# Performance work log

Hardware: AMD Instinct MI355X
Metric: run time of the kernel (lower is better)

Reference implementation:

```python
import jax, jax.numpy as jnp
import numpy as np
import math

B, S, D, H = 2, 2048, 1024, 16
DK = D // H


def setup_inputs() -> dict:
    key = jax.random.key(0)
    ks = jax.random.split(key, 10)
    sc = 1.0 / math.sqrt(D)
    inp = {
        "Q_input": jax.random.normal(ks[0], (B, S, D), dtype=jnp.float32),
        "Wq_w": jax.random.normal(ks[1], (D, D), dtype=jnp.float32) * sc,
        "Wq_b": jnp.zeros((D,), dtype=jnp.float32),
        "Wk_w": jax.random.normal(ks[2], (D, D), dtype=jnp.float32) * sc,
        "Wk_b": jnp.zeros((D,), dtype=jnp.float32),
        "Wv_w": jax.random.normal(ks[3], (D, D), dtype=jnp.float32) * sc,
        "Wv_b": jnp.zeros((D,), dtype=jnp.float32),
        "Wo_w": jax.random.normal(ks[4], (D, D), dtype=jnp.float32) * sc,
        "Wo_b": jnp.zeros((D,), dtype=jnp.float32),
        # causal mask, broadcast over batch and heads: [1,1,S,S]
        "mask": jnp.tril(jnp.ones((S, S), dtype=jnp.int32))[None, None],
    }
    return inp


def reference(Q_input, Wq_w, Wq_b, Wk_w, Wk_b, Wv_w, Wv_b, Wo_w, Wo_b, mask):
    b, s, _ = Q_input.shape
    # linear projections (torch Linear: x @ W^T + b)
    Q = Q_input @ Wq_w.T + Wq_b
    K = Q_input @ Wk_w.T + Wk_b
    V = Q_input @ Wv_w.T + Wv_b
    # [b, h, s, dk]
    Q = Q.reshape(b, s, H, DK).transpose(0, 2, 1, 3)
    K = K.reshape(b, s, H, DK).transpose(0, 2, 1, 3)
    V = V.reshape(b, s, H, DK).transpose(0, 2, 1, 3)
    scores = jnp.einsum("bhqd,bhkd->bhqk", Q, K) / math.sqrt(DK)
    scores = jnp.where(mask == 0, jnp.float32(-1e9), scores)
    weights = jax.nn.softmax(scores, axis=-1)
    attn = jnp.einsum("bhqk,bhkd->bhqd", weights, V)
    attn = attn.transpose(0, 2, 1, 3).reshape(b, s, D)
    return attn @ Wo_w.T + Wo_b
```

## Files before the change

kernel.cpp:

```cpp
#include <hip/hip_runtime.h>
#include <hip/hip_bf16.h>
#include <cstdint>

typedef __attribute__((ext_vector_type(8))) short short8;
typedef __attribute__((ext_vector_type(4))) float f32x4;
typedef __attribute__((ext_vector_type(2))) unsigned int uint2v;
typedef unsigned short ushort_t;

#define S_LEN 2048
#define D_DIM 1024
#define NH 16
#define DK 64
#define BATCH 2
#define M_ROWS (BATCH * S_LEN)
#define BK 32

__device__ inline ushort_t f2bf(float f) {
    union { float f; uint32_t u; } v; v.f = f;
    uint32_t r = v.u + 0x7fffu + ((v.u >> 16) & 1u);
    return (ushort_t)(r >> 16);
}

__device__ __forceinline__ ushort_t bfc(float f) {
    __hip_bfloat16 h = __float2bfloat16(f);
    return __builtin_bit_cast(ushort_t, h);
}

__device__ __forceinline__ void glds16(const ushort_t* g, ushort_t* l) {
    __builtin_amdgcn_global_load_lds(
        (const __attribute__((address_space(1))) uint32_t*)g,
        (__attribute__((address_space(3))) uint32_t*)l,
        16, 0, 0);
}

#if __has_builtin(__builtin_amdgcn_permlane16_swap) && __has_builtin(__builtin_amdgcn_permlane32_swap)
#define HAS_PLSWAP 1
#else
#define HAS_PLSWAP 0
#endif

__device__ __forceinline__ float red_max4(float x) {
#if HAS_PLSWAP
    uint2v a = __builtin_amdgcn_permlane16_swap(__float_as_uint(x), __float_as_uint(x), false, false);
    float y = fmaxf(__uint_as_float(a.x), __uint_as_float(a.y));
    uint2v b = __builtin_amdgcn_permlane32_swap(__float_as_uint(y), __float_as_uint(y), false, false);
    return fmaxf(__uint_as_float(b.x), __uint_as_float(b.y));
#else
    x = fmaxf(x, __shfl_xor(x, 16));
    return fmaxf(x, __shfl_xor(x, 32));
#endif
}
__device__ __forceinline__ float red_sum4(float x) {
#if HAS_PLSWAP
    uint2v a = __builtin_amdgcn_permlane16_swap(__float_as_uint(x), __float_as_uint(x), false, false);
    float y = __uint_as_float(a.x) + __uint_as_float(a.y);
    uint2v b = __builtin_amdgcn_permlane32_swap(__float_as_uint(y), __float_as_uint(y), false, false);
    return __uint_as_float(b.x) + __uint_as_float(b.y);
#else
    x += __shfl_xor(x, 16);
    return x + __shfl_xor(x, 32);
#endif
}

__device__ __forceinline__ void route_p(const uint32_t wp[4][2], int ks, int lane, uint32_t F[4]) {
#if HAS_PLSWAP
    uint32_t U0 = wp[2 * ks][0],     U1 = wp[2 * ks][1];
    uint32_t V0 = wp[2 * ks + 1][0], V1 = wp[2 * ks + 1][1];
    uint2v t, pa0, pa1, pb0, pb1;
    t = __builtin_amdgcn_permlane32_swap(U0, U0, false, false);
    pa0 = __builtin_amdgcn_permlane16_swap(U0, t.y, false, false);
    t = __builtin_amdgcn_permlane32_swap(U1, U1, false, false);
    pa1 = __builtin_amdgcn_permlane16_swap(U1, t.y, false, false);
    t = __builtin_amdgcn_permlane32_swap(V0, V0, false, false);
    pb0 = __builtin_amdgcn_permlane16_swap(t.x, V0, false, false);
    t = __builtin_amdgcn_permlane32_swap(V1, V1, false, false);
    pb1 = __builtin_amdgcn_permlane16_swap(t.x, V1, false, false);
    bool lo = lane < 32;
    F[0] = lo ? pa0.x : pb0.x;
    F[1] = lo ? pa1.x : pb1.x;
    F[2] = lo ? pa0.y : pb0.y;
    F[3] = lo ? pa1.y : pb1.y;
#else
    int q = lane & 15, g = lane >> 4;
#pragma unroll
    for (int m = 0; m < 4; m++) {
        int src = 16 * (2 * (g & 1) + (m >> 1)) + q;
        uint32_t xa = (uint32_t)__shfl((int)wp[2 * ks][m & 1], src);
        uint32_t xb = (uint32_t)__shfl((int)wp[2 * ks + 1][m & 1], src);
        F[m] = (g < 2) ? xa : xb;
    }
#endif
}

__global__ void cvt_bf16(const float* __restrict__ in, ushort_t* __restrict__ out, int n4) {
    int i = blockIdx.x * blockDim.x + threadIdx.x;
    int stride = gridDim.x * blockDim.x;
    for (int idx = i; idx < n4; idx += stride) {
        float4 v = ((const float4*)in)[idx];
        ushort4 o;
        o.x = f2bf(v.x); o.y = f2bf(v.y); o.z = f2bf(v.z); o.w = f2bf(v.w);
        ((ushort4*)out)[idx] = o;
    }
}

__global__ void cvt_w3(const float* __restrict__ wq, const float* __restrict__ wk,
                       const float* __restrict__ wv, ushort_t* __restrict__ wqkv) {
    const int seg = (D_DIM * D_DIM) / 4;
    int i = blockIdx.x * blockDim.x + threadIdx.x;
    int stride = gridDim.x * blockDim.x;
    for (int idx = i; idx < 3 * seg; idx += stride) {
        int sel = idx >> 18;
        int id = idx & (seg - 1);
        const float* src = sel == 0 ? wq : (sel == 1 ? wk : wv);
        float4 v = ((const float4*)src)[id];
        ushort4 o;
        o.x = f2bf(v.x); o.y = f2bf(v.y); o.z = f2bf(v.z); o.w = f2bf(v.w);
        ((ushort4*)wqkv)[sel * seg + id] = o;
    }
}

template<int MODE, int BMt, int BNt>
__global__ __launch_bounds__(256) void gemm_bt(const ushort_t* __restrict__ A,
                                               const ushort_t* __restrict__ Bw,
                                               const float* __restrict__ b0,
                                               const float* __restrict__ b1,
                                               const float* __restrict__ b2,
                                               void* __restrict__ C0,
                                               void* __restrict__ C1,
                                               void* __restrict__ C2,
                                               int M, int N, int K) {
    constexpr int FM = BMt / 32, FN = BNt / 32;
    constexpr int ACH = BMt / 64, BCH = BNt / 64;
    __shared__ ushort_t As[BMt * BK];
    __shared__ ushort_t Bs[BNt * BK];
    int tid = threadIdx.x;
    int lane = tid & 63;
    int w = tid >> 6;
    int wr = w >> 1, wc = w & 1;
    int nwg = gridDim.x;
    int bx = (blockIdx.x & 7) * (nwg >> 3) + (blockIdx.x >> 3);
    int ntile = N / BNt;
    int m0 = (bx / ntile) * BMt;
    int n0 = (bx % ntile) * BNt;
    int lr = lane & 15;
    int lk = (lane >> 4) * 8;
    int srow = lane >> 2;
    int scol = (lane & 3) * 8;

    f32x4 acc[FM][FN] = {};

    for (int kt = 0; kt < K; kt += BK) {
        __syncthreads();
#pragma unroll
        for (int c = 0; c < ACH; c++)
            glds16(&A[(size_t)(m0 + w * (BMt / 4) + c * 16 + srow) * K + kt + scol],
                   &As[(w * (BMt / 4) + c * 16) * BK]);
#pragma unroll
        for (int c = 0; c < BCH; c++)
            glds16(&Bw[(size_t)(n0 + w * (BNt / 4) + c * 16 + srow) * K + kt + scol],
                   &Bs[(w * (BNt / 4) + c * 16) * BK]);
        __syncthreads();

        short8 af[FM], bf[FN];
#pragma unroll
        for (int f = 0; f < FM; f++)
            af[f] = *(const short8*)&As[(wr * (BMt / 2) + f * 16 + lr) * BK + lk];
#pragma unroll
        for (int f = 0; f < FN; f++)
            bf[f] = *(const short8*)&Bs[(wc * (BNt / 2) + f * 16 + lr) * BK + lk];
#pragma unroll
        for (int i = 0; i < FM; i++)
#pragma unroll
            for (int j = 0; j < FN; j++)
                acc[i][j] = __builtin_amdgcn_mfma_f32_16x16x32_bf16(af[i], bf[j], acc[i][j], 0, 0, 0);
    }

    int r0 = (lane >> 4) * 4;
#pragma unroll
    for (int j = 0; j < FN; j++) {
        int ncol = n0 + wc * (BNt / 2) + j * 16 + lr;
        if (MODE == 2) {
            float bv = b0[ncol];
#pragma unroll
            for (int i = 0; i < FM; i++) {
                int mbase = m0 + wr * (BMt / 2) + i * 16 + r0;
#pragma unroll
                for (int r = 0; r < 4; r++)
                    ((float*)C0)[(size_t)(mbase + r) * N + ncol] = acc[i][j][r] + bv;
            }
        } else {
            int sel = n0 >> 10;
            const float* bp = sel == 0 ? b0 : (sel == 1 ? b1 : b2);
            int nc = ncol & 1023;
            float bv = bp[nc];
            int hh = nc >> 6, dk = nc & 63;
            ushort_t* Co = (ushort_t*)(sel == 0 ? C0 : (sel == 1 ? C1 : C2));
#pragma unroll
            for (int i = 0; i < FM; i++) {
                int mbase = m0 + wr * (BMt / 2) + i * 16 + r0;
                int bb = mbase >> 11, ss = mbase & 2047;
                if (sel == 2) {
                    ushort4 pk;
                    pk.x = f2bf(acc[i][j][0] + bv);
                    pk.y = f2bf(acc[i][j][1] + bv);
                    pk.z = f2bf(acc[i][j][2] + bv);
                    pk.w = f2bf(acc[i][j][3] + bv);
                    size_t idx = ((size_t)(bb * NH + hh) * DK + dk) * S_LEN + ss;
                    *(ushort4*)&Co[idx] = pk;
                } else {
#pragma unroll
                    for (int r = 0; r < 4; r++) {
                        size_t idx = ((size_t)(bb * NH + hh) * S_LEN + (ss + r)) * DK + dk;
                        Co[idx] = f2bf(acc[i][j][r] + bv);
                    }
                }
            }
        }
    }
}

#define CSC 0.1803368801f

__global__ __launch_bounds__(256) void attn_fwd(const ushort_t* __restrict__ Q,
                                                const ushort_t* __restrict__ K,
                                                const ushort_t* __restrict__ Vt,
                                                ushort_t* __restrict__ Oa) {
    __shared__ ushort_t Ks[2][64 * 64];
    __shared__ ushort_t Vs[2][64 * 64];

    int tid = threadIdx.x;
    int lane = tid & 63;
    int w = tid >> 6;
    int bh = blockIdx.x;
    int yy = blockIdx.y;
    int a = yy >> 3, bsel = yy & 7;
    int qt = (a == 0) ? bsel : (a == 1) ? 15 - bsel : (a == 2) ? 16 + bsel : 31 - bsel;
    size_t base = (size_t)bh * S_LEN * DK;
    int q0 = qt * 64;

    int lr = lane & 15;
    int lk = (lane >> 4) * 8;
    int g16 = (lane >> 4) * 16;
    int r0 = (lane >> 4) * 4;
    int wq = w * 16 + lr;

    auto swz = [](int row, int cb) { return (row * 128 + (cb ^ ((row & 7) << 4))) >> 1; };

    short8 qf0 = *(const short8*)&Q[base + (size_t)(q0 + wq) * DK + lk];
    short8 qf1 = *(const short8*)&Q[base + (size_t)(q0 + wq) * DK + 32 + lk];

    f32x4 o[4] = {};
    float mrowL = -1e30f, lrow = 0.f;

    int sr = tid >> 3;
    int scb = (tid & 7) * 16;
    int sce = (tid & 7) * 8;

    int NT = qt + 1;

    *(uint4*)&Ks[0][swz(sr, scb)]      = *(const uint4*)&K [base + (size_t)sr * DK + sce];
    *(uint4*)&Ks[0][swz(sr + 32, scb)] = *(const uint4*)&K [base + (size_t)(sr + 32) * DK + sce];
    *(uint4*)&Vs[0][swz(sr, scb)]      = *(const uint4*)&Vt[base + (size_t)sr * S_LEN + sce];
    *(uint4*)&Vs[0][swz(sr + 32, scb)] = *(const uint4*)&Vt[base + (size_t)(sr + 32) * S_LEN + sce];
    __syncthreads();

    int cur = 0;
    for (int t = 0; t < NT; ++t) {
        bool last = (t == NT - 1);
        bool diag = (t == qt);
        uint4 kr0, kr1, vr0, vr1;
        if (!last) {
            int tn = t + 1;
            kr0 = *(const uint4*)&K [base + (size_t)(tn * 64 + sr) * DK + sce];
            kr1 = *(const uint4*)&K [base + (size_t)(tn * 64 + sr + 32) * DK + sce];
            vr0 = *(const uint4*)&Vt[base + (size_t)sr * S_LEN + tn * 64 + sce];
            vr1 = *(const uint4*)&Vt[base + (size_t)(sr + 32) * S_LEN + tn * 64 + sce];
        }

        f32x4 st[4] = {};
        __builtin_amdgcn_s_setprio(1);
#pragma unroll
        for (int n = 0; n < 4; n++) {
            if (!diag || n <= w) {
                short8 kf0 = *(const short8*)&Ks[cur][swz(n * 16 + lr, g16)];
                short8 kf1 = *(const short8*)&Ks[cur][swz(n * 16 + lr, 64 + g16)];
                st[n] = __builtin_amdgcn_mfma_f32_16x16x32_bf16(kf0, qf0, st[n], 0, 0, 0);
                st[n] = __builtin_amdgcn_mfma_f32_16x16x32_bf16(kf1, qf1, st[n], 0, 0, 0);
            }
        }
        __builtin_amdgcn_s_setprio(0);

        if (diag) {
#pragma unroll
            for (int n = 0; n < 4; n++)
#pragma unroll
                for (int i = 0; i < 4; i++)
                    if (16 * n + r0 + i > wq) st[n][i] = -1e30f;
        }

        float mx = fmaxf(
            fmaxf(fmaxf(fmaxf(st[0][0], st[0][1]), fmaxf(st[0][2], st[0][3])),
                  fmaxf(fmaxf(st[1][0], st[1][1]), fmaxf(st[1][2], st[1][3]))),
            fmaxf(fmaxf(fmaxf(st[2][0], st[2][1]), fmaxf(st[2][2], st[2][3])),
                  fmaxf(fmaxf(st[3][0], st[3][1]), fmaxf(st[3][2], st[3][3]))));
        float mxL = red_max4(mx) * CSC;

        bool skip = __all(mxL <= mrowL + 8.0f);
        float corr = 1.0f;
        float mnewL = mrowL;
        if (!skip) {
            mnewL = fmaxf(mrowL, mxL);
            corr = exp2f(mrowL - mnewL);
            mrowL = mnewL;
        }

        float psum = 0.f;
        uint32_t wp[4][2];
#pragma unroll
        for (int n = 0; n < 4; n++) {
#pragma unroll
            for (int i = 0; i < 4; i++) {
                float p = exp2f(fmaf(st[n][i], CSC, -mnewL));
                st[n][i] = p;
                psum += p;
            }
            wp[n][0] = (uint32_t)bfc(st[n][0]) | ((uint32_t)bfc(st[n][1]) << 16);
            wp[n][1] = (uint32_t)bfc(st[n][2]) | ((uint32_t)bfc(st[n][3]) << 16);
        }
        psum = red_sum4(psum);

        if (skip) {
            lrow += psum;
        } else {
            lrow = lrow * corr + psum;
            float cb[4];
#pragma unroll
            for (int i = 0; i < 4; i++) cb[i] = __shfl(corr, r0 + i);
#pragma unroll
            for (int d = 0; d < 4; d++)
#pragma unroll
                for (int i = 0; i < 4; i++) o[d][i] *= cb[i];
        }

#pragma unroll
        for (int ks = 0; ks < 2; ks++) {
            if (diag && 32 * ks > w * 16 + 15) continue;
            uint32_t F[4];
            route_p(wp, ks, lane, F);
            union { uint32_t u[4]; short8 s; } pu;
            pu.u[0] = F[0]; pu.u[1] = F[1]; pu.u[2] = F[2]; pu.u[3] = F[3];
            short8 pf = pu.s;
            __builtin_amdgcn_s_setprio(1);
#pragma unroll
            for (int d = 0; d < 4; d++) {
                short8 vf = *(const short8*)&Vs[cur][swz(d * 16 + lr, ks * 64 + g16)];
                o[d] = __builtin_amdgcn_mfma_f32_16x16x32_bf16(pf, vf, o[d], 0, 0, 0);
            }
            __builtin_amdgcn_s_setprio(0);
        }

        if (!last) {
            *(uint4*)&Ks[cur ^ 1][swz(sr, scb)]      = kr0;
            *(uint4*)&Ks[cur ^ 1][swz(sr + 32, scb)] = kr1;
            *(uint4*)&Vs[cur ^ 1][swz(sr, scb)]      = vr0;
            *(uint4*)&Vs[cur ^ 1][swz(sr + 32, scb)] = vr1;
        }
        __syncthreads();
        cur ^= 1;
    }

    int b = bh >> 4, h = bh & 15;
    float lb[4];
#pragma unroll
    for (int i = 0; i < 4; i++) lb[i] = __shfl(lrow, r0 + i);
#pragma unroll
    for (int d = 0; d < 4; d++)
#pragma unroll
        for (int i = 0; i < 4; i++) {
            int qq = q0 + w * 16 + r0 + i;
            int dk = d * 16 + lr;
            size_t idx = ((size_t)(b * S_LEN + qq)) * D_DIM + h * DK + dk;
            Oa[idx] = bfc(o[d][i] / lb[i]);
        }
}

extern "C" void kernel_launch(void* const* d_in, const int* in_sizes, int n_in,
                              void* d_out, int out_size, void* d_ws, size_t ws_size,
                              hipStream_t stream) {
    const float* X  = (const float*)d_in[0];
    const float* Wq = (const float*)d_in[1];
    const float* bq = (const float*)d_in[2];
    const float* Wk = (const float*)d_in[3];
    const float* bk = (const float*)d_in[4];
    const float* Wv = (const float*)d_in[5];
    const float* bv = (const float*)d_in[6];
    const float* Wo = (const float*)d_in[7];
    const float* bo = (const float*)d_in[8];
    float* out = (float*)d_out;

    char* ws = (char*)d_ws;
    ushort_t* Xb    = (ushort_t*)ws;
    ushort_t* Wqkvb = (ushort_t*)(ws + (8u  << 20));
    ushort_t* Qb    = (ushort_t*)(ws + (14u << 20));
    ushort_t* Kb    = (ushort_t*)(ws + (22u << 20));
    ushort_t* Vtb   = (ushort_t*)(ws + (30u << 20));
    ushort_t* Wob   = Wqkvb;
    ushort_t* Ab    = Xb;

    const int M = M_ROWS;
    int nX4 = (M * D_DIM) / 4;
    int nW4 = (D_DIM * D_DIM) / 4;

    cvt_bf16<<<2048, 256, 0, stream>>>(X, Xb, nX4);
    cvt_w3<<<2048, 256, 0, stream>>>(Wq, Wk, Wv, Wqkvb);

    gemm_bt<3, 128, 128><<<dim3((M / 128) * (3072 / 128)), 256, 0, stream>>>(
        Xb, Wqkvb, bq, bk, bv, Qb, Kb, Vtb, M, 3072, D_DIM);

    cvt_bf16<<<2048, 256, 0, stream>>>(Wo, Wob, nW4);

    dim3 agrid(BATCH * NH, 32);
    attn_fwd<<<agrid, 256, 0, stream>>>(Qb, Kb, Vtb, Ab);

    gemm_bt<2, 64, 128><<<dim3((M / 64) * (D_DIM / 128)), 256, 0, stream>>>(
        Ab, Wob, bo, bo, bo, out, out, out, M, D_DIM, D_DIM);
}
```

Before: 133.1 us.

## Split long causal query tiles across two blocks and merge partial softmax results

The attention grid grows from 32 to 48 blocks per head. The 16 longest query tiles (rows 16-31) are each split into two key ranges handled by separate blocks, and the blocks are ordered through lookup tables to balance causal work. Partial outputs and (max, sum) statistics go to scratch buffers, reusing the weight workspace and the final output buffer. A new merge kernel combines them with log-sum-exp rescaling. This shortens the critical path of the heaviest blocks, at the cost of an extra launch, fp32 partial traffic, and a bf16 round trip on one partial. The Wo conversion is moved after the merge because its buffer is now reused.

```diff
diff --git a/kernel.cpp b/kernel.cpp
--- a/kernel.cpp
+++ b/kernel.cpp
@@ -24,6 +24,10 @@
 __device__ __forceinline__ ushort_t bfc(float f) {
     __hip_bfloat16 h = __float2bfloat16(f);
     return __builtin_bit_cast(ushort_t, h);
+}
+
+__device__ __forceinline__ float bf2f(ushort_t u) {
+    return __uint_as_float(((uint32_t)u) << 16);
 }
 
 __device__ __forceinline__ void glds16(const ushort_t* g, ushort_t* l) {
@@ -221,10 +225,27 @@
 
 #define CSC 0.1803368801f
 
+__device__ const unsigned char JTAB[48] = {
+    30,31,31,15,28,29,29,30,
+    25,24,13,28,27,27,26,14,
+    25,26,12,22,23,23,24,11,
+    19,19,18,10,22,21,21,20,
+    20, 9,16,17,17,18, 8,16,
+     0, 1, 2, 3, 4, 5, 6, 7};
+__device__ const unsigned char KTAB[48] = {
+     0, 0, 1, 9, 0, 0, 1, 1,
+     0, 0, 9, 1, 1, 0, 0, 9,
+     1, 1, 9, 0, 0, 1, 1, 9,
+     1, 0, 0, 9, 1, 1, 0, 0,
+     1, 9, 0, 0, 1, 1, 9, 1,
+     9, 9, 9, 9, 9, 9, 9, 9};
+
 __global__ __launch_bounds__(256) void attn_fwd(const ushort_t* __restrict__ Q,
                                                 const ushort_t* __restrict__ K,
                                                 const ushort_t* __restrict__ Vt,
-                                                ushort_t* __restrict__ Oa) {
+                                                ushort_t* __restrict__ Oa,
+                                                float2* __restrict__ ml,
+                                                float* __restrict__ Pd) {
     __shared__ ushort_t Ks[2][64 * 64];
     __shared__ ushort_t Vs[2][64 * 64];
 
@@ -233,10 +254,14 @@
     int w = tid >> 6;
     int bh = blockIdx.x;
     int yy = blockIdx.y;
-    int a = yy >> 3, bsel = yy & 7;
-    int qt = (a == 0) ? bsel : (a == 1) ? 15 - bsel : (a == 2) ? 16 + bsel : 31 - bsel;
+    int j = JTAB[yy];
+    int kk = KTAB[yy];
+    int nt = j + 1;
+    int half = (nt + 1) >> 1;
+    int t0 = (kk == 1) ? half : 0;
+    int t1 = (kk == 0) ? half : nt;
     size_t base = (size_t)bh * S_LEN * DK;
-    int q0 = qt * 64;
+    int q0 = j * 64;
 
     int lr = lane & 15;
     int lk = (lane >> 4) * 8;
@@ -256,18 +281,16 @@
     int scb = (tid & 7) * 16;
     int sce = (tid & 7) * 8;
 
-    int NT = qt + 1;
-
-    *(uint4*)&Ks[0][swz(sr, scb)]      = *(const uint4*)&K [base + (size_t)sr * DK + sce];
-    *(uint4*)&Ks[0][swz(sr + 32, scb)] = *(const uint4*)&K [base + (size_t)(sr + 32) * DK + sce];
-    *(uint4*)&Vs[0][swz(sr, scb)]      = *(const uint4*)&Vt[base + (size_t)sr * S_LEN + sce];
-    *(uint4*)&Vs[0][swz(sr + 32, scb)] = *(const uint4*)&Vt[base + (size_t)(sr + 32) * S_LEN + sce];
+    *(uint4*)&Ks[0][swz(sr, scb)]      = *(const uint4*)&K [base + (size_t)(t0 * 64 + sr) * DK + sce];
+    *(uint4*)&Ks[0][swz(sr + 32, scb)] = *(const uint4*)&K [base + (size_t)(t0 * 64 + sr + 32) * DK + sce];
+    *(uint4*)&Vs[0][swz(sr, scb)]      = *(const uint4*)&Vt[base + (size_t)sr * S_LEN + t0 * 64 + sce];
+    *(uint4*)&Vs[0][swz(sr + 32, scb)] = *(const uint4*)&Vt[base + (size_t)(sr + 32) * S_LEN + t0 * 64 + sce];
     __syncthreads();
 
     int cur = 0;
-    for (int t = 0; t < NT; ++t) {
-        bool last = (t == NT - 1);
-        bool diag = (t == qt);
+    for (int t = t0; t < t1; ++t) {
+        bool last = (t == t1 - 1);
+        bool diag = (t == j);
         uint4 kr0, kr1, vr0, vr1;
         if (!last) {
             int tn = t + 1;
@@ -370,18 +393,75 @@
     }
 
     int b = bh >> 4, h = bh & 15;
-    float lb[4];
-#pragma unroll
-    for (int i = 0; i < 4; i++) lb[i] = __shfl(lrow, r0 + i);
-#pragma unroll
-    for (int d = 0; d < 4; d++)
-#pragma unroll
-        for (int i = 0; i < 4; i++) {
-            int qq = q0 + w * 16 + r0 + i;
-            int dk = d * 16 + lr;
-            size_t idx = ((size_t)(b * S_LEN + qq)) * D_DIM + h * DK + dk;
-            Oa[idx] = bfc(o[d][i] / lb[i]);
-        }
+    if (kk == 9) {
+        float lb[4];
+#pragma unroll
+        for (int i = 0; i < 4; i++) lb[i] = __shfl(lrow, r0 + i);
+#pragma unroll
+        for (int d = 0; d < 4; d++)
+#pragma unroll
+            for (int i = 0; i < 4; i++) {
+                int qq = q0 + w * 16 + r0 + i;
+                int dk = d * 16 + lr;
+                size_t idx = ((size_t)(b * S_LEN + qq)) * D_DIM + h * DK + dk;
+                Oa[idx] = bfc(o[d][i] / lb[i]);
+            }
+    } else {
+        int jj = j - 16;
+        if (kk == 0) {
+#pragma unroll
+            for (int d = 0; d < 4; d++)
+#pragma unroll
+                for (int i = 0; i < 4; i++) {
+                    int qq = q0 + w * 16 + r0 + i;
+                    int dk = d * 16 + lr;
+                    size_t idx = ((size_t)(b * S_LEN + qq)) * D_DIM + h * DK + dk;
+                    Oa[idx] = bfc(o[d][i]);
+                }
+        } else {
+#pragma unroll
+            for (int d = 0; d < 4; d++)
+#pragma unroll
+                for (int i = 0; i < 4; i++) {
+                    int rloc = w * 16 + r0 + i;
+                    Pd[((size_t)(bh * 16 + jj) * 64 + rloc) * 64 + d * 16 + lr] = o[d][i];
+                }
+        }
+        if (lane < 16) {
+            int row = w * 16 + lane;
+            ml[(size_t)kk * 32768 + (bh * 16 + jj) * 64 + row] = make_float2(mrowL, lrow);
+        }
+    }
+}
+
+__global__ __launch_bounds__(256) void attn_merge(const float2* __restrict__ ml,
+                                                  const float* __restrict__ Pd,
+                                                  ushort_t* __restrict__ Oa) {
+    int bh = blockIdx.x;
+    int jj = blockIdx.y;
+    int tid = threadIdx.x;
+    int r = tid >> 2;
+    int q = (tid & 3) * 16;
+    int b = bh >> 4, h = bh & 15;
+    int row = (jj + 16) * 64 + r;
+    float2 a = ml[(bh * 16 + jj) * 64 + r];
+    float2 c = ml[32768 + (bh * 16 + jj) * 64 + r];
+    float M = fmaxf(a.x, c.x);
+    float w0 = exp2f(a.x - M), w1 = exp2f(c.x - M);
+    float rc = 1.0f / (a.y * w0 + c.y * w1);
+    size_t ob = ((size_t)(b * S_LEN + row)) * D_DIM + h * DK + q;
+    const float* p1 = &Pd[((size_t)(bh * 16 + jj) * 64 + r) * 64 + q];
+#pragma unroll
+    for (int i = 0; i < 4; i++) {
+        ushort4 o0 = *(const ushort4*)&Oa[ob + i * 4];
+        float4 o1 = *(const float4*)&p1[i * 4];
+        ushort4 res;
+        res.x = bfc((bf2f(o0.x) * w0 + o1.x * w1) * rc);
+        res.y = bfc((bf2f(o0.y) * w0 + o1.y * w1) * rc);
+        res.z = bfc((bf2f(o0.z) * w0 + o1.z * w1) * rc);
+        res.w = bfc((bf2f(o0.w) * w0 + o1.w * w1) * rc);
+        *(ushort4*)&Oa[ob + i * 4] = res;
+    }
 }
 
 extern "C" void kernel_launch(void* const* d_in, const int* in_sizes, int n_in,
@@ -401,11 +481,13 @@
     char* ws = (char*)d_ws;
     ushort_t* Xb    = (ushort_t*)ws;
     ushort_t* Wqkvb = (ushort_t*)(ws + (8u  << 20));
+    float2*   mlbuf = (float2*)(ws + (8u  << 20));
     ushort_t* Qb    = (ushort_t*)(ws + (14u << 20));
     ushort_t* Kb    = (ushort_t*)(ws + (22u << 20));
     ushort_t* Vtb   = (ushort_t*)(ws + (30u << 20));
     ushort_t* Wob   = Wqkvb;
     ushort_t* Ab    = Xb;
+    float*    Pd    = out;
 
     const int M = M_ROWS;
     int nX4 = (M * D_DIM) / 4;
@@ -417,10 +499,12 @@
     gemm_bt<3, 128, 128><<<dim3((M / 128) * (3072 / 128)), 256, 0, stream>>>(
         Xb, Wqkvb, bq, bk, bv, Qb, Kb, Vtb, M, 3072, D_DIM);
 
+    dim3 agrid(BATCH * NH, 48);
+    attn_fwd<<<agrid, 256, 0, stream>>>(Qb, Kb, Vtb, Ab, mlbuf, Pd);
+
+    attn_merge<<<dim3(BATCH * NH, 16), 256, 0, stream>>>(mlbuf, Pd, Ab);
+
     cvt_bf16<<<2048, 256, 0, stream>>>(Wo, Wob, nW4);
-
-    dim3 agrid(BATCH * NH, 32);
-    attn_fwd<<<agrid, 256, 0, stream>>>(Qb, Kb, Vtb, Ab);
 
     gemm_bt<2, 64, 128><<<dim3((M / 64) * (D_DIM / 128)), 256, 0, stream>>>(
         Ab, Wob, bo, bo, bo, out, out, out, M, D_DIM, D_DIM);
```

After: 133.7 us. Within noise of the previous version (+0.4%).
